# Optimization experiments

Hardware: AMD Instinct MI355X
Metric: run time of the kernel (lower is better)

Reference implementation:

```python
import jax, jax.numpy as jnp
import numpy as np

D_MODEL = 32   # channels arg = Mamba d_model
D_INNER = 32   # expand=1
D_STATE = 8
DT_RANK = 2    # ceil(32/16)
D_CONV = 4


def layer_norm(h, g, b, eps=1e-5):
    m = jnp.mean(h, axis=-1, keepdims=True)
    v = jnp.var(h, axis=-1, keepdims=True)
    return (h - m) * jax.lax.rsqrt(v + eps) * g + b


def causal_conv1d(h, w, b):
    # h: [B, d, L]; w: [d, K] depthwise; torch Conv1d(padding=K-1) truncated to first L
    out = jax.lax.conv_general_dilated(h, w[:, None, :], (1,), [(D_CONV - 1, 0)],
                                       dimension_numbers=('NCH', 'OIH', 'NCH'),
                                       feature_group_count=h.shape[1])
    return out + b[None, :, None]


def selective_scan(u, delta, A, Bm, Cm, D):
    # u, delta: [B, d, L]; A: [d, n]; Bm, Cm: [B, n, L]; D: [d]
    dA = jnp.exp(jnp.einsum('bdl,dn->lbdn', delta, A))       # [L, B, d, n]
    dBu = jnp.einsum('bdl,bnl,bdl->lbdn', delta, Bm, u)      # [L, B, d, n]
    Cseq = jnp.transpose(Cm, (2, 0, 1))                      # [L, B, n]
    h0 = jnp.zeros((u.shape[0], A.shape[0], A.shape[1]), u.dtype)

    def step(h, inp):
        dA_t, dBu_t, C_t = inp
        h = dA_t * h + dBu_t
        return h, jnp.einsum('bdn,bn->bd', h, C_t)

    _, ys = jax.lax.scan(step, h0, (dA, dBu, Cseq))          # ys: [L, B, d]
    return jnp.transpose(ys, (1, 2, 0)) + D[None, :, None] * u


def mamba_direction(xz, conv_w, conv_b, xproj_w, dtproj_w, dtproj_b, A_log, D):
    xh, z = jnp.split(xz, 2, axis=1)                         # each [B, d_inner, L]
    xh = jax.nn.silu(causal_conv1d(xh, conv_w, conv_b))
    x_dbl = jnp.einsum('bdl,kd->bkl', xh, xproj_w)           # [B, dt_rank+2n, L]
    dt, Bm, Cm = jnp.split(x_dbl, [DT_RANK, DT_RANK + D_STATE], axis=1)
    dt = jax.nn.softplus(jnp.einsum('brl,dr->bdl', dt, dtproj_w) + dtproj_b[None, :, None])
    y = selective_scan(xh, dt, -jnp.exp(A_log), Bm, Cm, D)
    return y * jax.nn.silu(z)


def forward(x, lin1_w, lin1_b, ln1_g, ln1_b, in_proj_w,
            conv_w_f, conv_b_f, xproj_w_f, dtproj_w_f, dtproj_b_f, A_log_f, D_f,
            conv_w_r, conv_b_r, xproj_w_r, dtproj_w_r, dtproj_b_r, A_log_r, D_r,
            out_proj_w, mnorm_g, mnorm_b, lin2_w, lin2_b):
    avg = jnp.mean(x, axis=(2, 3))                           # [B, C] adaptive avg pool
    mx = jnp.max(x, axis=(2, 3))                             # [B, C] adaptive max pool
    combined = jnp.stack([avg, mx], axis=-1)                 # [B, C, 2]
    h = combined @ lin1_w.T + lin1_b                         # [B, C, d_model]
    h = layer_norm(h, ln1_g, ln1_b)
    # bidirectional Mamba (bimamba v2) over sequence length L = C
    xz = jnp.einsum('blc,ec->bel', h, in_proj_w)             # [B, 2*d_inner, L]
    out_f = mamba_direction(xz, conv_w_f, conv_b_f, xproj_w_f, dtproj_w_f, dtproj_b_f, A_log_f, D_f)
    out_r = mamba_direction(xz[..., ::-1], conv_w_r, conv_b_r, xproj_w_r, dtproj_w_r, dtproj_b_r, A_log_r, D_r)[..., ::-1]
    out = (out_f + out_r) / 2.0                              # if_devide_out=True
    out = jnp.einsum('bdl,od->blo', out, out_proj_w)         # [B, L, d_model]
    out = layer_norm(out, mnorm_g, mnorm_b)                  # use_norm=True
    att = jax.nn.sigmoid(out @ lin2_w.T + lin2_b)            # [B, L, 1]
    return att[..., None] * 0.25 + 0.875                     # [B, C, 1, 1]


def setup_inputs() -> dict:
    key = jax.random.key(0)
    ks = jax.random.split(key, 12)
    B, C, H, W = 32, 512, 64, 64

    def rn(k, shape, s):
        return jax.random.normal(k, shape, jnp.float32) * s

    A_log = jnp.log(jnp.broadcast_to(jnp.arange(1, D_STATE + 1, dtype=jnp.float32), (D_INNER, D_STATE)))
    return {
        'x': jax.random.normal(ks[0], (B, C, H, W), jnp.float32),
        'lin1_w': rn(ks[1], (D_MODEL, 2), 0.5),
        'lin1_b': jnp.zeros((D_MODEL,), jnp.float32),
        'ln1_g': jnp.ones((D_MODEL,), jnp.float32),
        'ln1_b': jnp.zeros((D_MODEL,), jnp.float32),
        'in_proj_w': rn(ks[2], (2 * D_INNER, D_MODEL), 0.1),
        'conv_w_f': rn(ks[3], (D_INNER, D_CONV), 0.3),
        'conv_b_f': jnp.zeros((D_INNER,), jnp.float32),
        'xproj_w_f': rn(ks[4], (DT_RANK + 2 * D_STATE, D_INNER), 0.1),
        'dtproj_w_f': rn(ks[5], (D_INNER, DT_RANK), 0.5),
        'dtproj_b_f': jnp.full((D_INNER,), -4.6, jnp.float32),
        'A_log_f': A_log,
        'D_f': jnp.ones((D_INNER,), jnp.float32),
        'conv_w_r': rn(ks[6], (D_INNER, D_CONV), 0.3),
        'conv_b_r': jnp.zeros((D_INNER,), jnp.float32),
        'xproj_w_r': rn(ks[7], (DT_RANK + 2 * D_STATE, D_INNER), 0.1),
        'dtproj_w_r': rn(ks[8], (D_INNER, DT_RANK), 0.5),
        'dtproj_b_r': jnp.full((D_INNER,), -4.6, jnp.float32),
        'A_log_r': A_log,
        'D_r': jnp.ones((D_INNER,), jnp.float32),
        'out_proj_w': rn(ks[9], (D_MODEL, D_INNER), 0.1),
        'mnorm_g': jnp.ones((D_MODEL,), jnp.float32),
        'mnorm_b': jnp.zeros((D_MODEL,), jnp.float32),
        'lin2_w': rn(ks[10], (1, D_MODEL), 0.3),
        'lin2_b': jnp.zeros((1,), jnp.float32),
    }


def reference(x, lin1_w, lin1_b, ln1_g, ln1_b, in_proj_w,
              conv_w_f, conv_b_f, xproj_w_f, dtproj_w_f, dtproj_b_f, A_log_f, D_f,
              conv_w_r, conv_b_r, xproj_w_r, dtproj_w_r, dtproj_b_r, A_log_r, D_r,
              out_proj_w, mnorm_g, mnorm_b, lin2_w, lin2_b):
    return forward(x, lin1_w, lin1_b, ln1_g, ln1_b, in_proj_w,
                   conv_w_f, conv_b_f, xproj_w_f, dtproj_w_f, dtproj_b_f, A_log_f, D_f,
                   conv_w_r, conv_b_r, xproj_w_r, dtproj_w_r, dtproj_b_r, A_log_r, D_r,
                   out_proj_w, mnorm_g, mnorm_b, lin2_w, lin2_b)
```

## Files before the change

kernel.cpp:

```cpp
#include <hip/hip_runtime.h>
#include <math.h>

#define BB 32
#define CC 512
#define HW 4096
#define DM 32
#define DI 32
#define DS 8
#define KC 4

#define NCH 16
#define CHL 32

__device__ __forceinline__ float siluf(float x) {
    return x / (1.0f + __expf(-x));
}
__device__ __forceinline__ float softplusf(float x) {
    float ax = fabsf(x);
    return fmaxf(x, 0.0f) + log1pf(__expf(-ax));
}

__global__ __launch_bounds__(256) void poolproj_kernel(
    const float* __restrict__ x,
    const float* __restrict__ lin1_w, const float* __restrict__ lin1_b,
    const float* __restrict__ ln1_g, const float* __restrict__ ln1_b,
    const float* __restrict__ in_proj_w, float* __restrict__ xz)
{
    __shared__ float sWp[64][33];
    int tid = threadIdx.x;
    for (int i = tid; i < 64 * DM; i += 256) sWp[i >> 5][i & 31] = in_proj_w[i];
    __syncthreads();

    int wave = tid >> 6, lane = tid & 63;
    int row = blockIdx.x * 4 + wave;
    const float4* xp = reinterpret_cast<const float4*>(x + (size_t)row * HW);
    float s = 0.f, m = -INFINITY;
#pragma unroll
    for (int k = 0; k < 16; ++k) {
        float4 v = xp[k * 64 + lane];
        s += (v.x + v.y) + (v.z + v.w);
        m = fmaxf(m, fmaxf(fmaxf(v.x, v.y), fmaxf(v.z, v.w)));
    }
#pragma unroll
    for (int off = 1; off < 64; off <<= 1) {
        s += __shfl_xor(s, off);
        m = fmaxf(m, __shfl_xor(m, off));
    }
    float a = s * (1.0f / HW);
    int m_ = lane & 31;
    float h = a * lin1_w[2 * m_] + m * lin1_w[2 * m_ + 1] + lin1_b[m_];
    float sum = h;
#pragma unroll
    for (int mask = 1; mask < 32; mask <<= 1) sum += __shfl_xor(sum, mask);
    float mean = sum * (1.0f / DM);
    float d = h - mean;
    float vs = d * d;
#pragma unroll
    for (int mask = 1; mask < 32; mask <<= 1) vs += __shfl_xor(vs, mask);
    float rs = rsqrtf(vs * (1.0f / DM) + 1e-5f);
    float hn = d * rs * ln1_g[m_] + ln1_b[m_];
    float acc = 0.f;
#pragma unroll
    for (int mm = 0; mm < DM; ++mm)
        acc += __shfl(hn, mm) * sWp[lane][mm];
    xz[((size_t)row << 6) + lane] = acc;
}

__global__ __launch_bounds__(256) void convscan1_kernel(
    const float* __restrict__ xz,
    const float* __restrict__ conv_w_f, const float* __restrict__ conv_b_f,
    const float* __restrict__ xproj_w_f, const float* __restrict__ dtproj_w_f,
    const float* __restrict__ dtproj_b_f,
    const float* __restrict__ conv_w_r, const float* __restrict__ conv_b_r,
    const float* __restrict__ xproj_w_r, const float* __restrict__ dtproj_w_r,
    const float* __restrict__ dtproj_b_r,
    const float* __restrict__ A_log_f, const float* __restrict__ A_log_r,
    float* __restrict__ u_g, float* __restrict__ dt_g,
    float* __restrict__ B_g, float* __restrict__ C_g,
    float* __restrict__ carrA, float* __restrict__ carrH)
{
    int bx = blockIdx.x;
    int bd = bx >> 4, j = bx & 15;
    int b = bd >> 1, dir = bd & 1;
    int tid = threadIdx.x;
    const float* cw = dir ? conv_w_r : conv_w_f;
    const float* cb = dir ? conv_b_r : conv_b_f;
    const float* xw = dir ? xproj_w_r : xproj_w_f;
    const float* dw = dir ? dtproj_w_r : dtproj_w_f;
    const float* db = dir ? dtproj_b_r : dtproj_b_f;
    const float* Alog = dir ? A_log_r : A_log_f;

    __shared__ float xt[32][39];
    __shared__ float xw_s[18][33];
    __shared__ float u_s[CHL][33];
    __shared__ float dt_s[CHL][33];
    __shared__ float B_s[CHL][9];
    __shared__ float C_s[CHL][9];
    __shared__ float dtr_s[CHL][2];

    for (int idx = tid; idx < 35 * 32; idx += 256) {
        int t = idx >> 5, dd = idx & 31;
        int sidx = j * CHL - 3 + t;
        float v = 0.f;
        if (sidx >= 0) {
            int orig = dir ? (511 - sidx) : sidx;
            v = xz[(((size_t)b * 512 + orig) << 6) + dd];
        }
        xt[dd][t] = v;
    }
    for (int idx = tid; idx < 18 * 32; idx += 256)
        xw_s[idx >> 5][idx & 31] = xw[idx];
    __syncthreads();

    int l = tid >> 3, g8 = tid & 7;
#pragma unroll
    for (int i = 0; i < 4; ++i) {
        int dd = g8 * 4 + i;
        float acc = cb[dd];
#pragma unroll
        for (int k = 0; k < KC; ++k) acc += cw[dd * KC + k] * xt[dd][l + k];
        u_s[l][dd] = siluf(acc);
    }
    __syncthreads();

    for (int o = g8; o < 18; o += 8) {
        float acc = 0.f;
#pragma unroll
        for (int m_ = 0; m_ < 32; ++m_) acc += u_s[l][m_] * xw_s[o][m_];
        if (o < 2) dtr_s[l][o] = acc;
        else if (o < 10) B_s[l][o - 2] = acc;
        else             C_s[l][o - 10] = acc;
    }
    __syncthreads();

    size_t rowbase = ((size_t)bd * 512 + j * CHL) * 32;
    for (int idx = tid; idx < CHL * 32; idx += 256) {
        int ll = idx >> 5, dd = idx & 31;
        float v = dtr_s[ll][0] * dw[dd * 2] + dtr_s[ll][1] * dw[dd * 2 + 1] + db[dd];
        float sp = softplusf(v);
        dt_s[ll][dd] = sp;
        dt_g[rowbase + idx] = sp;
        u_g[rowbase + idx] = u_s[ll][dd];
    }
    size_t base8 = ((size_t)bd * 512 + j * CHL) * 8;
    if (tid < CHL * 8) {
        B_g[base8 + tid] = B_s[tid >> 3][tid & 7];
        C_g[base8 + tid] = C_s[tid >> 3][tid & 7];
    }
    __syncthreads();

    int dd = tid >> 3, nn = tid & 7;
    float Aa = -__expf(Alog[tid]);
    float ap = 1.f, h = 0.f;
#pragma unroll 4
    for (int sl = 0; sl < CHL; ++sl) {
        float dtv = dt_s[sl][dd];
        float uu  = u_s[sl][dd];
        float bm  = B_s[sl][nn];
        float dA  = __expf(dtv * Aa);
        ap *= dA;
        h = dA * h + dtv * uu * bm;
    }
    carrA[((size_t)bx << 8) + tid] = ap;
    carrH[((size_t)bx << 8) + tid] = h;
}

__global__ __launch_bounds__(512) void scan2final_kernel(
    const float* __restrict__ u_g, const float* __restrict__ dt_g,
    const float* __restrict__ B_g, const float* __restrict__ C_g,
    const float* __restrict__ carrA, const float* __restrict__ carrH,
    const float* __restrict__ A_log_f, const float* __restrict__ D_f,
    const float* __restrict__ A_log_r, const float* __restrict__ D_r,
    const float* __restrict__ xz,
    const float* __restrict__ out_proj_w, const float* __restrict__ mnorm_g,
    const float* __restrict__ mnorm_b, const float* __restrict__ lin2_w,
    const float* __restrict__ lin2_b, float* __restrict__ out)
{
    int bx = blockIdx.x;
    int b = bx >> 4, t = bx & 15;
    int tid = threadIdx.x;
    int L0 = t * CHL;

    __shared__ float u_s[2][CHL][33];
    __shared__ float dt_s[2][CHL][33];
    __shared__ float B_s[2][CHL][12];
    __shared__ float C_s[2][CHL][12];
    __shared__ float z_s[CHL][33];
    __shared__ float y_s[2][CHL][33];
    __shared__ float comb_s[CHL][33];
    __shared__ float opw_s[DM][33];

    for (int idx = tid; idx < 2 * CHL * 32; idx += 512) {
        int dirw = idx >> 10;
        int r2 = idx & 1023;
        int sl = r2 >> 5, d = r2 & 31;
        int bd = b * 2 + dirw;
        int tc = dirw ? (15 - t) : t;
        size_t g = ((size_t)bd * 512 + tc * CHL + sl) * 32 + d;
        u_s[dirw][sl][d]  = u_g[g];
        dt_s[dirw][sl][d] = dt_g[g];
    }
    {
        int dirw = tid >> 8;
        int r2 = tid & 255;
        int sl = r2 >> 3, n = r2 & 7;
        int bd = b * 2 + dirw;
        int tc = dirw ? (15 - t) : t;
        size_t g = ((size_t)bd * 512 + tc * CHL + sl) * 8 + n;
        B_s[dirw][sl][n] = B_g[g];
        C_s[dirw][sl][n] = C_g[g];
    }
    for (int idx = tid; idx < CHL * 32; idx += 512) {
        int l = idx >> 5, d = idx & 31;
        z_s[l][d] = xz[(((size_t)b * 512 + L0 + l) << 6) + 32 + d];
        opw_s[idx >> 5][d] = out_proj_w[idx];
    }
    __syncthreads();

    {
        int dir = tid >> 8;
        int r = tid & 255;
        int d = r >> 3, n = r & 7;
        int bd = b * 2 + dir;
        int tt = dir ? (15 - t) : t;
        const float* Alog = dir ? A_log_r : A_log_f;
        const float* Dp   = dir ? D_r : D_f;
        float A  = -__expf(Alog[r]);
        float Dd = Dp[d];

        float h = 0.f;
        for (int g4 = 0; g4 < 4; ++g4) {
            int jbase = g4 * 4;
            if (jbase >= tt) break;
            float av[4], hv[4];
#pragma unroll
            for (int k = 0; k < 4; ++k) {
                int jj = jbase + k;
                int js = (jj < tt) ? jj : 0;
                size_t cb2 = (((size_t)bd * NCH + js) << 8) + r;
                av[k] = carrA[cb2];
                hv[k] = carrH[cb2];
            }
#pragma unroll
            for (int k = 0; k < 4; ++k)
                if (jbase + k < tt) h = av[k] * h + hv[k];
        }

#pragma unroll 4
        for (int sl = 0; sl < CHL; ++sl) {
            float dtv = dt_s[dir][sl][d];
            float uu  = u_s[dir][sl][d];
            float bm  = B_s[dir][sl][n];
            float cm  = C_s[dir][sl][n];
            h = __expf(dtv * A) * h + dtv * uu * bm;
            float py = h * cm;
            py += __shfl_xor(py, 1);
            py += __shfl_xor(py, 2);
            py += __shfl_xor(py, 4);
            if (n == 0) {
                int ll = dir ? (CHL - 1 - sl) : sl;
                y_s[dir][ll][d] = py + Dd * uu;
            }
        }
    }
    __syncthreads();

    for (int idx = tid; idx < CHL * 32; idx += 512) {
        int l = idx >> 5, d = idx & 31;
        comb_s[l][d] = 0.5f * (y_s[0][l][d] + y_s[1][l][d]) * siluf(z_s[l][d]);
    }
    __syncthreads();

    {
        int l = tid >> 4, k = tid & 15;
        float oa = 0.f, ob = 0.f;
#pragma unroll
        for (int d = 0; d < DI; ++d) {
            float c = comb_s[l][d];
            oa += c * opw_s[k][d];
            ob += c * opw_s[k + 16][d];
        }
        float sum = oa + ob;
#pragma unroll
        for (int mask = 1; mask < 16; mask <<= 1) sum += __shfl_xor(sum, mask);
        float mean = sum * (1.0f / DM);
        float da = oa - mean, db2 = ob - mean;
        float vs = da * da + db2 * db2;
#pragma unroll
        for (int mask = 1; mask < 16; mask <<= 1) vs += __shfl_xor(vs, mask);
        float rs = rsqrtf(vs * (1.0f / DM) + 1e-5f);
        float va = da * rs * mnorm_g[k] + mnorm_b[k];
        float vb = db2 * rs * mnorm_g[k + 16] + mnorm_b[k + 16];
        float sv = va * lin2_w[k] + vb * lin2_w[k + 16];
#pragma unroll
        for (int mask = 1; mask < 16; mask <<= 1) sv += __shfl_xor(sv, mask);
        if (k == 0) {
            float att = 1.0f / (1.0f + __expf(-(sv + lin2_b[0])));
            out[(size_t)b * 512 + L0 + l] = 0.25f * att + 0.875f;
        }
    }
}

extern "C" void kernel_launch(void* const* d_in, const int* in_sizes, int n_in,
                              void* d_out, int out_size, void* d_ws, size_t ws_size,
                              hipStream_t stream)
{
    const float* x         = (const float*)d_in[0];
    const float* lin1_w    = (const float*)d_in[1];
    const float* lin1_b    = (const float*)d_in[2];
    const float* ln1_g     = (const float*)d_in[3];
    const float* ln1_b     = (const float*)d_in[4];
    const float* in_proj_w = (const float*)d_in[5];
    const float* conv_w_f  = (const float*)d_in[6];
    const float* conv_b_f  = (const float*)d_in[7];
    const float* xproj_w_f = (const float*)d_in[8];
    const float* dtproj_w_f= (const float*)d_in[9];
    const float* dtproj_b_f= (const float*)d_in[10];
    const float* A_log_f   = (const float*)d_in[11];
    const float* D_f       = (const float*)d_in[12];
    const float* conv_w_r  = (const float*)d_in[13];
    const float* conv_b_r  = (const float*)d_in[14];
    const float* xproj_w_r = (const float*)d_in[15];
    const float* dtproj_w_r= (const float*)d_in[16];
    const float* dtproj_b_r= (const float*)d_in[17];
    const float* A_log_r   = (const float*)d_in[18];
    const float* D_r       = (const float*)d_in[19];
    const float* out_proj_w= (const float*)d_in[20];
    const float* mnorm_g   = (const float*)d_in[21];
    const float* mnorm_b   = (const float*)d_in[22];
    const float* lin2_w    = (const float*)d_in[23];
    const float* lin2_b    = (const float*)d_in[24];

    float* ws   = (float*)d_ws;
    float* xz   = ws;
    float* u_g  = xz + 1048576;
    float* dt_g = u_g + 1048576;
    float* B_g  = dt_g + 1048576;
    float* C_g  = B_g + 262144;
    float* carrA= C_g + 262144;
    float* carrH= carrA + 262144;
    (void)ws_size; (void)in_sizes; (void)n_in; (void)out_size;

    poolproj_kernel<<<4096, 256, 0, stream>>>(x, lin1_w, lin1_b, ln1_g, ln1_b, in_proj_w, xz);
    convscan1_kernel<<<BB * 2 * NCH, 256, 0, stream>>>(
        xz, conv_w_f, conv_b_f, xproj_w_f, dtproj_w_f, dtproj_b_f,
        conv_w_r, conv_b_r, xproj_w_r, dtproj_w_r, dtproj_b_r,
        A_log_f, A_log_r, u_g, dt_g, B_g, C_g, carrA, carrH);
    scan2final_kernel<<<BB * NCH, 512, 0, stream>>>(
        u_g, dt_g, B_g, C_g, carrA, carrH,
        A_log_f, D_f, A_log_r, D_r, xz,
        out_proj_w, mnorm_g, mnorm_b, lin2_w, lin2_b, (float*)d_out);
}
```

Baseline: 76.47 us.

## Fuse conv/scan and final-scan kernels into one cooperative kernel with grid sync

Merges the chunk-local conv/projection/scan kernel and the carry-combine/output kernel into a single cooperative launch. Each block computes both directions for one chunk and keeps u, dt, B and C in shared memory across a grid-wide barrier, so those intermediates no longer round-trip through global memory. The cost is a grid sync and a cooperative launch, which needs all 512 blocks to be co-resident. The heavier shared-memory footprint may limit occupancy.

Measured after the change: 182.4 us. 139% more time.

```diff
diff --git a/kernel.cpp b/kernel.cpp
--- a/kernel.cpp
+++ b/kernel.cpp
@@ -1,5 +1,8 @@
 #include <hip/hip_runtime.h>
+#include <hip/hip_cooperative_groups.h>
 #include <math.h>
+
+namespace cg = cooperative_groups;
 
 #define BB 32
 #define CC 512
@@ -66,7 +69,7 @@
     xz[((size_t)row << 6) + lane] = acc;
 }
 
-__global__ __launch_bounds__(256) void convscan1_kernel(
+__global__ __launch_bounds__(512, 4) void coopscan_kernel(
     const float* __restrict__ xz,
     const float* __restrict__ conv_w_f, const float* __restrict__ conv_b_f,
     const float* __restrict__ xproj_w_f, const float* __restrict__ dtproj_w_f,
@@ -74,142 +77,104 @@
     const float* __restrict__ conv_w_r, const float* __restrict__ conv_b_r,
     const float* __restrict__ xproj_w_r, const float* __restrict__ dtproj_w_r,
     const float* __restrict__ dtproj_b_r,
-    const float* __restrict__ A_log_f, const float* __restrict__ A_log_r,
-    float* __restrict__ u_g, float* __restrict__ dt_g,
-    float* __restrict__ B_g, float* __restrict__ C_g,
-    float* __restrict__ carrA, float* __restrict__ carrH)
-{
-    int bx = blockIdx.x;
-    int bd = bx >> 4, j = bx & 15;
-    int b = bd >> 1, dir = bd & 1;
-    int tid = threadIdx.x;
-    const float* cw = dir ? conv_w_r : conv_w_f;
-    const float* cb = dir ? conv_b_r : conv_b_f;
-    const float* xw = dir ? xproj_w_r : xproj_w_f;
-    const float* dw = dir ? dtproj_w_r : dtproj_w_f;
-    const float* db = dir ? dtproj_b_r : dtproj_b_f;
-    const float* Alog = dir ? A_log_r : A_log_f;
-
-    __shared__ float xt[32][39];
-    __shared__ float xw_s[18][33];
-    __shared__ float u_s[CHL][33];
-    __shared__ float dt_s[CHL][33];
-    __shared__ float B_s[CHL][9];
-    __shared__ float C_s[CHL][9];
-    __shared__ float dtr_s[CHL][2];
-
-    for (int idx = tid; idx < 35 * 32; idx += 256) {
-        int t = idx >> 5, dd = idx & 31;
-        int sidx = j * CHL - 3 + t;
-        float v = 0.f;
-        if (sidx >= 0) {
-            int orig = dir ? (511 - sidx) : sidx;
-            v = xz[(((size_t)b * 512 + orig) << 6) + dd];
-        }
-        xt[dd][t] = v;
-    }
-    for (int idx = tid; idx < 18 * 32; idx += 256)
-        xw_s[idx >> 5][idx & 31] = xw[idx];
-    __syncthreads();
-
-    int l = tid >> 3, g8 = tid & 7;
-#pragma unroll
-    for (int i = 0; i < 4; ++i) {
-        int dd = g8 * 4 + i;
-        float acc = cb[dd];
-#pragma unroll
-        for (int k = 0; k < KC; ++k) acc += cw[dd * KC + k] * xt[dd][l + k];
-        u_s[l][dd] = siluf(acc);
-    }
-    __syncthreads();
-
-    for (int o = g8; o < 18; o += 8) {
-        float acc = 0.f;
-#pragma unroll
-        for (int m_ = 0; m_ < 32; ++m_) acc += u_s[l][m_] * xw_s[o][m_];
-        if (o < 2) dtr_s[l][o] = acc;
-        else if (o < 10) B_s[l][o - 2] = acc;
-        else             C_s[l][o - 10] = acc;
-    }
-    __syncthreads();
-
-    size_t rowbase = ((size_t)bd * 512 + j * CHL) * 32;
-    for (int idx = tid; idx < CHL * 32; idx += 256) {
-        int ll = idx >> 5, dd = idx & 31;
-        float v = dtr_s[ll][0] * dw[dd * 2] + dtr_s[ll][1] * dw[dd * 2 + 1] + db[dd];
-        float sp = softplusf(v);
-        dt_s[ll][dd] = sp;
-        dt_g[rowbase + idx] = sp;
-        u_g[rowbase + idx] = u_s[ll][dd];
-    }
-    size_t base8 = ((size_t)bd * 512 + j * CHL) * 8;
-    if (tid < CHL * 8) {
-        B_g[base8 + tid] = B_s[tid >> 3][tid & 7];
-        C_g[base8 + tid] = C_s[tid >> 3][tid & 7];
-    }
-    __syncthreads();
-
-    int dd = tid >> 3, nn = tid & 7;
-    float Aa = -__expf(Alog[tid]);
-    float ap = 1.f, h = 0.f;
-#pragma unroll 4
-    for (int sl = 0; sl < CHL; ++sl) {
-        float dtv = dt_s[sl][dd];
-        float uu  = u_s[sl][dd];
-        float bm  = B_s[sl][nn];
-        float dA  = __expf(dtv * Aa);
-        ap *= dA;
-        h = dA * h + dtv * uu * bm;
-    }
-    carrA[((size_t)bx << 8) + tid] = ap;
-    carrH[((size_t)bx << 8) + tid] = h;
-}
-
-__global__ __launch_bounds__(512) void scan2final_kernel(
-    const float* __restrict__ u_g, const float* __restrict__ dt_g,
-    const float* __restrict__ B_g, const float* __restrict__ C_g,
-    const float* __restrict__ carrA, const float* __restrict__ carrH,
     const float* __restrict__ A_log_f, const float* __restrict__ D_f,
     const float* __restrict__ A_log_r, const float* __restrict__ D_r,
-    const float* __restrict__ xz,
     const float* __restrict__ out_proj_w, const float* __restrict__ mnorm_g,
     const float* __restrict__ mnorm_b, const float* __restrict__ lin2_w,
-    const float* __restrict__ lin2_b, float* __restrict__ out)
+    const float* __restrict__ lin2_b,
+    float* __restrict__ carrA, float* __restrict__ carrH,
+    float* __restrict__ out)
 {
     int bx = blockIdx.x;
     int b = bx >> 4, t = bx & 15;
     int tid = threadIdx.x;
     int L0 = t * CHL;
 
+    __shared__ float xt[2][32][39];
+    __shared__ float xw_s[2][18][33];
+    __shared__ float dtr_s[2][CHL][2];
     __shared__ float u_s[2][CHL][33];
     __shared__ float dt_s[2][CHL][33];
-    __shared__ float B_s[2][CHL][12];
-    __shared__ float C_s[2][CHL][12];
+    __shared__ float B_s[2][CHL][9];
+    __shared__ float C_s[2][CHL][9];
     __shared__ float z_s[CHL][33];
     __shared__ float y_s[2][CHL][33];
     __shared__ float comb_s[CHL][33];
     __shared__ float opw_s[DM][33];
 
-    for (int idx = tid; idx < 2 * CHL * 32; idx += 512) {
-        int dirw = idx >> 10;
-        int r2 = idx & 1023;
-        int sl = r2 >> 5, d = r2 & 31;
-        int bd = b * 2 + dirw;
-        int tc = dirw ? (15 - t) : t;
-        size_t g = ((size_t)bd * 512 + tc * CHL + sl) * 32 + d;
-        u_s[dirw][sl][d]  = u_g[g];
-        dt_s[dirw][sl][d] = dt_g[g];
-    }
     {
-        int dirw = tid >> 8;
-        int r2 = tid & 255;
-        int sl = r2 >> 3, n = r2 & 7;
-        int bd = b * 2 + dirw;
-        int tc = dirw ? (15 - t) : t;
-        size_t g = ((size_t)bd * 512 + tc * CHL + sl) * 8 + n;
-        B_s[dirw][sl][n] = B_g[g];
-        C_s[dirw][sl][n] = C_g[g];
-    }
+        int dir = tid >> 8;
+        int tid2 = tid & 255;
+        int j = dir ? (15 - t) : t;
+        const float* cw = dir ? conv_w_r : conv_w_f;
+        const float* cb = dir ? conv_b_r : conv_b_f;
+        const float* xw = dir ? xproj_w_r : xproj_w_f;
+        const float* dw = dir ? dtproj_w_r : dtproj_w_f;
+        const float* db = dir ? dtproj_b_r : dtproj_b_f;
+        const float* Alog = dir ? A_log_r : A_log_f;
+
+        for (int idx = tid2; idx < 35 * 32; idx += 256) {
+            int tc = idx >> 5, dd = idx & 31;
+            int sidx = j * CHL - 3 + tc;
+            float v = 0.f;
+            if (sidx >= 0) {
+                int orig = dir ? (511 - sidx) : sidx;
+                v = xz[(((size_t)b * 512 + orig) << 6) + dd];
+            }
+            xt[dir][dd][tc] = v;
+        }
+        for (int idx = tid2; idx < 18 * 32; idx += 256)
+            xw_s[dir][idx >> 5][idx & 31] = xw[idx];
+        __syncthreads();
+
+        int l = tid2 >> 3, g8 = tid2 & 7;
+#pragma unroll
+        for (int i = 0; i < 4; ++i) {
+            int dd = g8 * 4 + i;
+            float acc = cb[dd];
+#pragma unroll
+            for (int k = 0; k < KC; ++k) acc += cw[dd * KC + k] * xt[dir][dd][l + k];
+            u_s[dir][l][dd] = siluf(acc);
+        }
+        __syncthreads();
+
+        for (int o = g8; o < 18; o += 8) {
+            float acc = 0.f;
+#pragma unroll
+            for (int m_ = 0; m_ < 32; ++m_) acc += u_s[dir][l][m_] * xw_s[dir][o][m_];
+            if (o < 2) dtr_s[dir][l][o] = acc;
+            else if (o < 10) B_s[dir][l][o - 2] = acc;
+            else             C_s[dir][l][o - 10] = acc;
+        }
+        __syncthreads();
+
+        for (int idx = tid2; idx < CHL * 32; idx += 256) {
+            int ll = idx >> 5, dd = idx & 31;
+            float v = dtr_s[dir][ll][0] * dw[dd * 2] + dtr_s[dir][ll][1] * dw[dd * 2 + 1] + db[dd];
+            dt_s[dir][ll][dd] = softplusf(v);
+        }
+        __syncthreads();
+
+        int dd = tid2 >> 3, nn = tid2 & 7;
+        float Aa = -__expf(Alog[tid2]);
+        float ap = 1.f, h = 0.f;
+#pragma unroll 4
+        for (int sl = 0; sl < CHL; ++sl) {
+            float dtv = dt_s[dir][sl][dd];
+            float uu  = u_s[dir][sl][dd];
+            float bm  = B_s[dir][sl][nn];
+            float dA  = __expf(dtv * Aa);
+            ap *= dA;
+            h = dA * h + dtv * uu * bm;
+        }
+        size_t cidx = (((size_t)(b * 2 + dir) * NCH + j) << 8) + tid2;
+        carrA[cidx] = ap;
+        carrH[cidx] = h;
+    }
+
+    __threadfence();
+    cg::this_grid().sync();
+
     for (int idx = tid; idx < CHL * 32; idx += 512) {
         int l = idx >> 5, d = idx & 31;
         z_s[l][d] = xz[(((size_t)b * 512 + L0 + l) << 6) + 32 + d];
@@ -333,21 +298,21 @@
 
     float* ws   = (float*)d_ws;
     float* xz   = ws;
-    float* u_g  = xz + 1048576;
-    float* dt_g = u_g + 1048576;
-    float* B_g  = dt_g + 1048576;
-    float* C_g  = B_g + 262144;
-    float* carrA= C_g + 262144;
+    float* carrA= xz + 1048576;
     float* carrH= carrA + 262144;
+    float* outp = (float*)d_out;
     (void)ws_size; (void)in_sizes; (void)n_in; (void)out_size;
 
     poolproj_kernel<<<4096, 256, 0, stream>>>(x, lin1_w, lin1_b, ln1_g, ln1_b, in_proj_w, xz);
-    convscan1_kernel<<<BB * 2 * NCH, 256, 0, stream>>>(
-        xz, conv_w_f, conv_b_f, xproj_w_f, dtproj_w_f, dtproj_b_f,
-        conv_w_r, conv_b_r, xproj_w_r, dtproj_w_r, dtproj_b_r,
-        A_log_f, A_log_r, u_g, dt_g, B_g, C_g, carrA, carrH);
-    scan2final_kernel<<<BB * NCH, 512, 0, stream>>>(
-        u_g, dt_g, B_g, C_g, carrA, carrH,
-        A_log_f, D_f, A_log_r, D_r, xz,
-        out_proj_w, mnorm_g, mnorm_b, lin2_w, lin2_b, (float*)d_out);
-}
+
+    void* args[] = {
+        (void*)&xz,
+        (void*)&conv_w_f, (void*)&conv_b_f, (void*)&xproj_w_f, (void*)&dtproj_w_f, (void*)&dtproj_b_f,
+        (void*)&conv_w_r, (void*)&conv_b_r, (void*)&xproj_w_r, (void*)&dtproj_w_r, (void*)&dtproj_b_r,
+        (void*)&A_log_f, (void*)&D_f, (void*)&A_log_r, (void*)&D_r,
+        (void*)&out_proj_w, (void*)&mnorm_g, (void*)&mnorm_b, (void*)&lin2_w, (void*)&lin2_b,
+        (void*)&carrA, (void*)&carrH, (void*)&outp
+    };
+    hipLaunchCooperativeKernel((const void*)coopscan_kernel, dim3(BB * NCH), dim3(512),
+                               args, 0, stream);
+}
```

## Process both scan directions in one block sharing a single xz tile load

Applied to the files above, without the earlier changes.

The conv+chunk-scan kernel now handles the forward and reverse directions of the same sequence chunk in one 512-thread block instead of two separate 256-thread blocks. The xz tile is loaded once, with a 3-element halo on both sides, and the reverse direction reads it with mirrored conv taps. Chunk outputs are written back to the reversed positions and chunk indices. This halves redundant global loads of xz and halves the block count. In exchange, shared memory per block and per-block register pressure rise, and the reverse direction's global writes are scattered in mirrored order.

Result: no change. 76.90 us (+0.6%).

```diff
diff --git a/kernel.cpp b/kernel.cpp
--- a/kernel.cpp
+++ b/kernel.cpp
@@ -66,7 +66,7 @@
     xz[((size_t)row << 6) + lane] = acc;
 }
 
-__global__ __launch_bounds__(256) void convscan1_kernel(
+__global__ __launch_bounds__(512) void convscan1_kernel(
     const float* __restrict__ xz,
     const float* __restrict__ conv_w_f, const float* __restrict__ conv_b_f,
     const float* __restrict__ xproj_w_f, const float* __restrict__ dtproj_w_f,
@@ -80,89 +80,121 @@
     float* __restrict__ carrA, float* __restrict__ carrH)
 {
     int bx = blockIdx.x;
-    int bd = bx >> 4, j = bx & 15;
-    int b = bd >> 1, dir = bd & 1;
+    int b = bx >> 4, t = bx & 15;
     int tid = threadIdx.x;
-    const float* cw = dir ? conv_w_r : conv_w_f;
-    const float* cb = dir ? conv_b_r : conv_b_f;
-    const float* xw = dir ? xproj_w_r : xproj_w_f;
-    const float* dw = dir ? dtproj_w_r : dtproj_w_f;
-    const float* db = dir ? dtproj_b_r : dtproj_b_f;
-    const float* Alog = dir ? A_log_r : A_log_f;
-
-    __shared__ float xt[32][39];
-    __shared__ float xw_s[18][33];
-    __shared__ float u_s[CHL][33];
-    __shared__ float dt_s[CHL][33];
-    __shared__ float B_s[CHL][9];
-    __shared__ float C_s[CHL][9];
-    __shared__ float dtr_s[CHL][2];
-
-    for (int idx = tid; idx < 35 * 32; idx += 256) {
-        int t = idx >> 5, dd = idx & 31;
-        int sidx = j * CHL - 3 + t;
+    int L0 = t * CHL;
+
+    __shared__ float xt[32][41];
+    __shared__ float xw_s[2][18][33];
+    __shared__ float u_s[2][CHL][33];
+    __shared__ float dt_s[2][CHL][33];
+    __shared__ float B_s[2][CHL][9];
+    __shared__ float C_s[2][CHL][9];
+    __shared__ float dtr_s[2][CHL][2];
+
+    for (int idx = tid; idx < 38 * 32; idx += 512) {
+        int c = idx >> 5, dd = idx & 31;
+        int col = L0 - 3 + c;
         float v = 0.f;
-        if (sidx >= 0) {
-            int orig = dir ? (511 - sidx) : sidx;
-            v = xz[(((size_t)b * 512 + orig) << 6) + dd];
-        }
-        xt[dd][t] = v;
-    }
-    for (int idx = tid; idx < 18 * 32; idx += 256)
-        xw_s[idx >> 5][idx & 31] = xw[idx];
-    __syncthreads();
-
-    int l = tid >> 3, g8 = tid & 7;
-#pragma unroll
-    for (int i = 0; i < 4; ++i) {
-        int dd = g8 * 4 + i;
-        float acc = cb[dd];
-#pragma unroll
-        for (int k = 0; k < KC; ++k) acc += cw[dd * KC + k] * xt[dd][l + k];
-        u_s[l][dd] = siluf(acc);
-    }
-    __syncthreads();
-
-    for (int o = g8; o < 18; o += 8) {
-        float acc = 0.f;
-#pragma unroll
-        for (int m_ = 0; m_ < 32; ++m_) acc += u_s[l][m_] * xw_s[o][m_];
-        if (o < 2) dtr_s[l][o] = acc;
-        else if (o < 10) B_s[l][o - 2] = acc;
-        else             C_s[l][o - 10] = acc;
-    }
-    __syncthreads();
-
-    size_t rowbase = ((size_t)bd * 512 + j * CHL) * 32;
-    for (int idx = tid; idx < CHL * 32; idx += 256) {
-        int ll = idx >> 5, dd = idx & 31;
-        float v = dtr_s[ll][0] * dw[dd * 2] + dtr_s[ll][1] * dw[dd * 2 + 1] + db[dd];
-        float sp = softplusf(v);
-        dt_s[ll][dd] = sp;
-        dt_g[rowbase + idx] = sp;
-        u_g[rowbase + idx] = u_s[ll][dd];
-    }
-    size_t base8 = ((size_t)bd * 512 + j * CHL) * 8;
-    if (tid < CHL * 8) {
-        B_g[base8 + tid] = B_s[tid >> 3][tid & 7];
-        C_g[base8 + tid] = C_s[tid >> 3][tid & 7];
-    }
-    __syncthreads();
-
-    int dd = tid >> 3, nn = tid & 7;
-    float Aa = -__expf(Alog[tid]);
-    float ap = 1.f, h = 0.f;
+        if (col >= 0 && col < 512)
+            v = xz[(((size_t)b * 512 + col) << 6) + dd];
+        xt[dd][c] = v;
+    }
+    for (int idx = tid; idx < 2 * 18 * 32; idx += 512) {
+        int dirw = idx >= 576;
+        int r2 = idx - dirw * 576;
+        const float* xw = dirw ? xproj_w_r : xproj_w_f;
+        xw_s[dirw][r2 >> 5][r2 & 31] = xw[r2];
+    }
+    __syncthreads();
+
+#pragma unroll
+    for (int p = 0; p < 4; ++p) {
+        int idx = p * 512 + tid;
+        int dd = idx & 31, l = (idx >> 5) & 31, dirw = idx >> 10;
+        const float* cw2 = dirw ? conv_w_r : conv_w_f;
+        const float* cb2 = dirw ? conv_b_r : conv_b_f;
+        float acc = cb2[dd];
+        if (dirw == 0) {
+#pragma unroll
+            for (int k = 0; k < KC; ++k) acc += cw2[dd * KC + k] * xt[dd][l + k];
+        } else {
+#pragma unroll
+            for (int jj = 0; jj < KC; ++jj) acc += cw2[dd * KC + 3 - jj] * xt[dd][l + 3 + jj];
+        }
+        u_s[dirw][l][dd] = siluf(acc);
+    }
+    __syncthreads();
+
+#pragma unroll
+    for (int p = 0; p < 3; ++p) {
+        int idx = p * 512 + tid;
+        if (idx < 1152) {
+            int dirw = idx >= 576;
+            int r2 = idx - dirw * 576;
+            int o = r2 >> 5, l = r2 & 31;
+            float acc = 0.f;
+#pragma unroll
+            for (int m_ = 0; m_ < 32; ++m_) acc += u_s[dirw][l][m_] * xw_s[dirw][o][m_];
+            if (o < 2)       dtr_s[dirw][l][o] = acc;
+            else if (o < 10) B_s[dirw][l][o - 2] = acc;
+            else             C_s[dirw][l][o - 10] = acc;
+        }
+    }
+    __syncthreads();
+
+#pragma unroll
+    for (int p = 0; p < 4; ++p) {
+        int idx = p * 512 + tid;
+        int dd = idx & 31, l = (idx >> 5) & 31, dirw = idx >> 10;
+        const float* dw2 = dirw ? dtproj_w_r : dtproj_w_f;
+        const float* db2 = dirw ? dtproj_b_r : dtproj_b_f;
+        float v = dtr_s[dirw][l][0] * dw2[dd * 2] + dtr_s[dirw][l][1] * dw2[dd * 2 + 1] + db2[dd];
+        dt_s[dirw][l][dd] = softplusf(v);
+    }
+    __syncthreads();
+
+#pragma unroll
+    for (int p = 0; p < 4; ++p) {
+        int idx = p * 512 + tid;
+        int dd = idx & 31, l = (idx >> 5) & 31, dirw = idx >> 10;
+        int sp = dirw ? (511 - (L0 + l)) : (L0 + l);
+        size_t g = ((size_t)(b * 2 + dirw) * 512 + sp) * 32 + dd;
+        u_g[g]  = u_s[dirw][l][dd];
+        dt_g[g] = dt_s[dirw][l][dd];
+    }
+    {
+        int dirw = tid >> 8;
+        int r2 = tid & 255;
+        int l = r2 >> 3, n = r2 & 7;
+        int sp = dirw ? (511 - (L0 + l)) : (L0 + l);
+        size_t g = ((size_t)(b * 2 + dirw) * 512 + sp) * 8 + n;
+        B_g[g] = B_s[dirw][l][n];
+        C_g[g] = C_s[dirw][l][n];
+    }
+
+    {
+        int dir = tid >> 8;
+        int tid2 = tid & 255;
+        int dd = tid2 >> 3, nn = tid2 & 7;
+        int jc = dir ? (15 - t) : t;
+        const float* Alog = dir ? A_log_r : A_log_f;
+        float Aa = -__expf(Alog[tid2]);
+        float ap = 1.f, h = 0.f;
 #pragma unroll 4
-    for (int sl = 0; sl < CHL; ++sl) {
-        float dtv = dt_s[sl][dd];
-        float uu  = u_s[sl][dd];
-        float bm  = B_s[sl][nn];
-        float dA  = __expf(dtv * Aa);
-        ap *= dA;
-        h = dA * h + dtv * uu * bm;
-    }
-    carrA[((size_t)bx << 8) + tid] = ap;
-    carrH[((size_t)bx << 8) + tid] = h;
+        for (int sl = 0; sl < CHL; ++sl) {
+            int ll = dir ? (CHL - 1 - sl) : sl;
+            float dtv = dt_s[dir][ll][dd];
+            float uu  = u_s[dir][ll][dd];
+            float bm  = B_s[dir][ll][nn];
+            float dA  = __expf(dtv * Aa);
+            ap *= dA;
+            h = dA * h + dtv * uu * bm;
+        }
+        size_t cidx = (((size_t)(b * 2 + dir) * NCH + jc) << 8) + tid2;
+        carrA[cidx] = ap;
+        carrH[cidx] = h;
+    }
 }
 
 __global__ __launch_bounds__(512) void scan2final_kernel(
@@ -342,7 +374,7 @@
     (void)ws_size; (void)in_sizes; (void)n_in; (void)out_size;
 
     poolproj_kernel<<<4096, 256, 0, stream>>>(x, lin1_w, lin1_b, ln1_g, ln1_b, in_proj_w, xz);
-    convscan1_kernel<<<BB * 2 * NCH, 256, 0, stream>>>(
+    convscan1_kernel<<<BB * NCH, 512, 0, stream>>>(
         xz, conv_w_f, conv_b_f, xproj_w_f, dtproj_w_f, dtproj_b_f,
         conv_w_r, conv_b_r, xproj_w_r, dtproj_w_r, dtproj_b_r,
         A_log_f, A_log_r, u_g, dt_g, B_g, C_g, carrA, carrH);
```
